# Kernel tuning notes

Measured on AMD Instinct MI355X. Metric: run time of the kernel, lower is better.

## Reference

```python
import jax, jax.numpy as jnp
import numpy as np

B, S, D, H = 4, 4096, 1024, 1024


def log_g(x):
    # where(x >= 0, log(relu(x) + 0.5), -softplus(-x)); relu(x)+0.5 >= 0.5 so log is safe
    return jnp.where(x >= 0, jnp.log(jax.nn.relu(x) + 0.5), -jax.nn.softplus(-x))


def setup_inputs() -> dict:
    key = jax.random.key(0)
    ks = jax.random.split(key, 8)
    scale = 1.0 / np.sqrt(D)
    return {
        "x_t": jax.random.normal(ks[0], (B, S, D), dtype=jnp.float32),
        "pre_h": jax.random.normal(ks[1], (B, 1, H), dtype=jnp.float32),
        "W_f": jax.random.uniform(ks[2], (H, D), jnp.float32, -scale, scale),
        "b_f": jax.random.uniform(ks[3], (H,), jnp.float32, -scale, scale),
        "W_i": jax.random.uniform(ks[4], (H, D), jnp.float32, -scale, scale),
        "b_i": jax.random.uniform(ks[5], (H,), jnp.float32, -scale, scale),
        "W_h": jax.random.uniform(ks[6], (H, D), jnp.float32, -scale, scale),
        "b_h": jax.random.uniform(ks[7], (H,), jnp.float32, -scale, scale),
    }


def reference(x_t, pre_h, W_f, b_f, W_i, b_i, W_h, b_h):
    sp = jax.nn.softplus
    f_pre = jnp.einsum("bsd,hd->bsh", x_t, W_f) + b_f
    i_pre = jnp.einsum("bsd,hd->bsh", x_t, W_i) + b_i
    h_pre = jnp.einsum("bsd,hd->bsh", x_t, W_h) + b_h

    diff = sp(-f_pre) - sp(-i_pre)
    log_f = -sp(diff)        # (B, S, H)
    log_i = -sp(-diff)       # (B, S, H)

    log_h0 = log_g(pre_h)                 # (B, 1, H)
    log_tilde_h = log_g(h_pre)            # (B, S, H)
    log_values = jnp.concatenate([log_h0, log_i + log_tilde_h], axis=1)  # (B, S+1, H)

    # parallel_scan_log: pad cumsum at END of seq dim (as in source: F.pad(..., (0,0,0,1)))
    a_star = jnp.pad(jnp.cumsum(log_f, axis=1), ((0, 0), (0, 1), (0, 0)))  # (B, S+1, H)
    log_h0_plus_b_star = jax.lax.cumlogsumexp(log_values - a_star, axis=1)
    log_h = a_star + log_h0_plus_b_star
    return jnp.exp(log_h)[:, 1:]  # (B, S, H)
```

## Files before the change

### kernel.cpp

```cpp
#include <hip/hip_runtime.h>
#include <hip/hip_bf16.h>
#include <math.h>

#define B_DIM 4
#define S_DIM 4096
#define K_DIM 1024
#define H_DIM 1024
#define M_DIM (B_DIM * S_DIM)

#define BMT 128
#define BNT 64
#define KT_ITERS (K_DIM / 32)

#define NCHUNK 64
#define CLEN (S_DIM / NCHUNK)

typedef __attribute__((ext_vector_type(8))) _Float16 f16x8;
typedef __attribute__((ext_vector_type(4))) _Float16 f16x4;
typedef __attribute__((ext_vector_type(4))) float f32x4;

__device__ __forceinline__ float sp_f(float x) {
    return fmaxf(x, 0.0f) + __logf(1.0f + __expf(-fabsf(x)));
}
__device__ __forceinline__ float log_g_f(float x) {
    return (x >= 0.0f) ? __logf(x + 0.5f) : -sp_f(-x);
}
__device__ __forceinline__ float logaddexp_f(float a, float b) {
    float m = fmaxf(a, b);
    return m + __logf(1.0f + __expf(-fabsf(a - b)));
}
__device__ __forceinline__ float exp_sat(float x) {
    return __expf(fminf(x, 85.0f));
}

__device__ __forceinline__ void gl_lds16(const void* g, void* l) {
    __builtin_amdgcn_global_load_lds(
        (const __attribute__((address_space(1))) unsigned int*)g,
        (__attribute__((address_space(3))) unsigned int*)l, 16, 0, 0);
}

__global__ __launch_bounds__(256) void conv_f16(
    const float* __restrict__ src, _Float16* __restrict__ dst, int n4)
{
    int i = blockIdx.x * 256 + threadIdx.x;
    if (i >= n4) return;
    float4 v = ((const float4*)src)[i];
    f16x4 o = {(_Float16)v.x, (_Float16)v.y, (_Float16)v.z, (_Float16)v.w};
    ((f16x4*)dst)[i] = o;
}

__global__ __launch_bounds__(256, 3) void gemm3(
    const _Float16* __restrict__ xh,
    const _Float16* __restrict__ wh,
    const float* __restrict__ bfp, const float* __restrict__ bip,
    const float* __restrict__ bhp,
    _Float16* __restrict__ lf_out, _Float16* __restrict__ w_out)
{
    __shared__ __align__(16) char smem[20480];

    const int tid = threadIdx.x;
    const int lane = tid & 63;
    const int wv = tid >> 6;
    const int wm = wv >> 1;
    const int wn = wv & 1;

    const int row0 = blockIdx.y * BMT;
    const int col0 = blockIdx.x * BNT;

    const int arow = tid & 127, akq = tid >> 7;
    unsigned ga0 = (unsigned)(((row0 + arow) * K_DIM + akq * 8) * 2);
    const int brow = tid & 63, bkq = tid >> 6;
    unsigned gb0 = (unsigned)(((0 * H_DIM + col0 + brow) * K_DIM + bkq * 8) * 2);
    unsigned gb1 = (unsigned)(((1 * H_DIM + col0 + brow) * K_DIM + bkq * 8) * 2);
    unsigned gb2 = (unsigned)(((2 * H_DIM + col0 + brow) * K_DIM + bkq * 8) * 2);

    const char* __restrict__ px = (const char*)xh;
    const char* __restrict__ pw = (const char*)wh;

    int aoff[4], boff[2];
#pragma unroll
    for (int mi = 0; mi < 4; ++mi)
        aoff[mi] = ((lane >> 4) << 11) + ((wm * 64 + mi * 16 + (lane & 15)) << 4);
#pragma unroll
    for (int nj = 0; nj < 2; ++nj)
        boff[nj] = ((lane >> 4) << 10) + ((wn * 32 + nj * 16 + (lane & 15)) << 4);

    f32x4 acc[3][4][2];
#pragma unroll
    for (int g = 0; g < 3; ++g)
#pragma unroll
        for (int mi = 0; mi < 4; ++mi)
#pragma unroll
            for (int nj = 0; nj < 2; ++nj)
                acc[g][mi][nj] = (f32x4){0.f, 0.f, 0.f, 0.f};

    for (int kt = 0; kt < KT_ITERS; ++kt) {
        __syncthreads();
        gl_lds16(px + ga0, smem + tid * 16);
        gl_lds16(px + ga0 + 32, smem + 4096 + tid * 16);
        gl_lds16(pw + gb0, smem + 8192 + tid * 16);
        gl_lds16(pw + gb1, smem + 12288 + tid * 16);
        gl_lds16(pw + gb2, smem + 16384 + tid * 16);
        ga0 += 64; gb0 += 64; gb1 += 64; gb2 += 64;
        __syncthreads();

        f16x8 a[4];
#pragma unroll
        for (int mi = 0; mi < 4; ++mi)
            a[mi] = *(const f16x8*)(smem + aoff[mi]);
#pragma unroll
        for (int g = 0; g < 3; ++g) {
            const char* bb = smem + 8192 + g * 4096;
            f16x8 b0 = *(const f16x8*)(bb + boff[0]);
            f16x8 b1 = *(const f16x8*)(bb + boff[1]);
#pragma unroll
            for (int mi = 0; mi < 4; ++mi) {
                acc[g][mi][0] = __builtin_amdgcn_mfma_f32_16x16x32_f16(a[mi], b0, acc[g][mi][0], 0, 0, 0);
                acc[g][mi][1] = __builtin_amdgcn_mfma_f32_16x16x32_f16(a[mi], b1, acc[g][mi][1], 0, 0, 0);
            }
        }
    }

    int nidx[2];
    float bfv[2], biv[2], bhv[2];
#pragma unroll
    for (int nj = 0; nj < 2; ++nj) {
        nidx[nj] = col0 + wn * 32 + nj * 16 + (lane & 15);
        bfv[nj] = bfp[nidx[nj]];
        biv[nj] = bip[nidx[nj]];
        bhv[nj] = bhp[nidx[nj]];
    }
#pragma unroll
    for (int mi = 0; mi < 4; ++mi) {
#pragma unroll
        for (int r = 0; r < 4; ++r) {
            int m = row0 + wm * 64 + mi * 16 + ((lane >> 4) << 2) + r;
#pragma unroll
            for (int nj = 0; nj < 2; ++nj) {
                float f_pre = acc[0][mi][nj][r] + bfv[nj];
                float i_pre = acc[1][mi][nj][r] + biv[nj];
                float h_pre = acc[2][mi][nj][r] + bhv[nj];
                float diff = sp_f(-f_pre) - sp_f(-i_pre);
                float lfv = -sp_f(diff);
                float wv_ = -sp_f(-diff) + log_g_f(h_pre);
                size_t o = (size_t)m * H_DIM + nidx[nj];
                lf_out[o] = (_Float16)lfv;
                w_out[o] = (_Float16)wv_;
            }
        }
    }
}

__global__ __launch_bounds__(256) void scan_pass_a(
    const _Float16* __restrict__ lf, const _Float16* __restrict__ w,
    float2* __restrict__ agg)
{
    int tid = blockIdx.x * blockDim.x + threadIdx.x;
    int h = tid & (H_DIM - 1);
    int b = (tid >> 10) & (B_DIM - 1);
    int q = tid >> 12;

    int tstart = q * CLEN + 1;
    int tend = (q == NCHUNK - 1) ? (S_DIM - 1) : (q * CLEN + CLEN);

    size_t idx = (size_t)(b * S_DIM + tstart) * H_DIM + h;
    float c = 0.0f, r = -INFINITY;
    for (int t = tstart; t <= tend; ++t) {
        c += (float)lf[idx];
        r = logaddexp_f(r, (float)w[idx - H_DIM] - c);
        idx += H_DIM;
    }
    agg[(size_t)(b * H_DIM + h) * NCHUNK + q] = make_float2(c, r);
}

__global__ __launch_bounds__(256) void scan_pass_b(
    const _Float16* __restrict__ lf, const float* __restrict__ preh,
    const float2* __restrict__ agg, float2* __restrict__ prefix)
{
    int col = blockIdx.x * blockDim.x + threadIdx.x;
    int h = col & (H_DIM - 1);
    int b = col >> 10;

    float lf0 = (float)lf[(size_t)(b * S_DIM) * H_DIM + h];
    float C = lf0;
    float R = log_g_f(preh[b * H_DIM + h]) - lf0;
    for (int q = 0; q < NCHUNK; ++q) {
        prefix[(size_t)col * NCHUNK + q] = make_float2(C, R);
        float2 a = agg[(size_t)col * NCHUNK + q];
        float Rn = logaddexp_f(R, a.y - C);
        C += a.x;
        R = Rn;
    }
}

__global__ __launch_bounds__(256) void scan_pass_c(
    const _Float16* __restrict__ lf, const _Float16* __restrict__ w,
    const float2* __restrict__ prefix, float* __restrict__ out)
{
    int tid = blockIdx.x * blockDim.x + threadIdx.x;
    int h = tid & (H_DIM - 1);
    int b = (tid >> 10) & (B_DIM - 1);
    int q = tid >> 12;

    float2 p = prefix[(size_t)(b * H_DIM + h) * NCHUNK + q];
    float C = p.x, R = p.y;

    int tstart = q * CLEN + 1;
    int tend = (q == NCHUNK - 1) ? (S_DIM - 1) : (q * CLEN + CLEN);

    size_t idx = (size_t)(b * S_DIM + tstart) * H_DIM + h;
    for (int t = tstart; t <= tend; ++t) {
        C += (float)lf[idx];
        R = logaddexp_f(R, (float)w[idx - H_DIM] - C);
        out[idx - H_DIM] = exp_sat(C + R);
        idx += H_DIM;
    }
    if (q == NCHUNK - 1) {
        R = logaddexp_f(R, (float)w[idx - H_DIM]);
        out[idx - H_DIM] = exp_sat(R);
    }
}

extern "C" void kernel_launch(void* const* d_in, const int* in_sizes, int n_in,
                              void* d_out, int out_size, void* d_ws, size_t ws_size,
                              hipStream_t stream) {
    const float* x    = (const float*)d_in[0];
    const float* preh = (const float*)d_in[1];
    const float* Wf   = (const float*)d_in[2];
    const float* bf   = (const float*)d_in[3];
    const float* Wi   = (const float*)d_in[4];
    const float* bi   = (const float*)d_in[5];
    const float* Wh   = (const float*)d_in[6];
    const float* bh   = (const float*)d_in[7];
    float* out = (float*)d_out;

    _Float16* xh = (_Float16*)d_ws;
    _Float16* wh = xh + (size_t)M_DIM * K_DIM;
    _Float16* lf = wh + (size_t)3 * H_DIM * K_DIM;
    _Float16* wbuf = lf + (size_t)M_DIM * H_DIM;
    float2* agg = (float2*)(wbuf + (size_t)M_DIM * H_DIM);
    float2* prefix = agg + (size_t)B_DIM * H_DIM * NCHUNK;

    conv_f16<<<(M_DIM * K_DIM / 4) / 256, 256, 0, stream>>>(x, xh, M_DIM * K_DIM / 4);
    conv_f16<<<(H_DIM * K_DIM / 4) / 256, 256, 0, stream>>>(Wf, wh, H_DIM * K_DIM / 4);
    conv_f16<<<(H_DIM * K_DIM / 4) / 256, 256, 0, stream>>>(
        Wi, wh + (size_t)H_DIM * K_DIM, H_DIM * K_DIM / 4);
    conv_f16<<<(H_DIM * K_DIM / 4) / 256, 256, 0, stream>>>(
        Wh, wh + (size_t)2 * H_DIM * K_DIM, H_DIM * K_DIM / 4);

    gemm3<<<dim3(H_DIM / BNT, M_DIM / BMT), 256, 0, stream>>>(
        xh, wh, bf, bi, bh, lf, wbuf);

    scan_pass_a<<<(B_DIM * H_DIM * NCHUNK) / 256, 256, 0, stream>>>(lf, wbuf, agg);
    scan_pass_b<<<(B_DIM * H_DIM) / 256, 256, 0, stream>>>(lf, preh, agg, prefix);
    scan_pass_c<<<(B_DIM * H_DIM * NCHUNK) / 256, 256, 0, stream>>>(lf, wbuf, prefix, out);
}
```

Before: 393.0 us.

## Interleave lf/w buffers, widen scan to two columns, double GEMM K tile, fuse conversions

Merges the four fp16 conversion launches into one kernel. Doubles the GEMM K tile per iteration to 64, halving the barrier count at the cost of twice the LDS. Stores log_f and the log-value term interleaved as half2 in a single buffer. The scan passes now handle two hidden columns per thread with wider loads and stores, and carry the previous w value in a register instead of reloading it. These changes target launch overhead, synchronization and memory transaction efficiency, though fewer threads in the scan passes and higher LDS use may reduce occupancy.

```diff
diff --git a/kernel.cpp b/kernel.cpp
--- a/kernel.cpp
+++ b/kernel.cpp
@@ -1,5 +1,4 @@
 #include <hip/hip_runtime.h>
-#include <hip/hip_bf16.h>
 #include <math.h>
 
 #define B_DIM 4
@@ -10,13 +9,16 @@
 
 #define BMT 128
 #define BNT 64
-#define KT_ITERS (K_DIM / 32)
+#define BKT 64
+#define KT_ITERS (K_DIM / BKT)
 
 #define NCHUNK 64
 #define CLEN (S_DIM / NCHUNK)
+#define HP (H_DIM / 2)
 
 typedef __attribute__((ext_vector_type(8))) _Float16 f16x8;
 typedef __attribute__((ext_vector_type(4))) _Float16 f16x4;
+typedef __attribute__((ext_vector_type(2))) _Float16 f16x2;
 typedef __attribute__((ext_vector_type(4))) float f32x4;
 
 __device__ __forceinline__ float sp_f(float x) {
@@ -39,14 +41,22 @@
         (__attribute__((address_space(3))) unsigned int*)l, 16, 0, 0);
 }
 
-__global__ __launch_bounds__(256) void conv_f16(
-    const float* __restrict__ src, _Float16* __restrict__ dst, int n4)
+#define N4X (M_DIM * K_DIM / 4)
+#define N4W (H_DIM * K_DIM / 4)
+__global__ __launch_bounds__(256) void conv_all(
+    const float* __restrict__ x, const float* __restrict__ Wf,
+    const float* __restrict__ Wi, const float* __restrict__ Wh,
+    _Float16* __restrict__ dst)
 {
     int i = blockIdx.x * 256 + threadIdx.x;
-    if (i >= n4) return;
-    float4 v = ((const float4*)src)[i];
-    f16x4 o = {(_Float16)v.x, (_Float16)v.y, (_Float16)v.z, (_Float16)v.w};
-    ((f16x4*)dst)[i] = o;
+    const float* src; int off;
+    if (i < N4X)              { src = x;  off = i; }
+    else if (i < N4X + N4W)   { src = Wf; off = i - N4X; }
+    else if (i < N4X + 2*N4W) { src = Wi; off = i - N4X - N4W; }
+    else                      { src = Wh; off = i - N4X - 2*N4W; }
+    float4 v = ((const float4*)src)[off];
+    ((f16x4*)dst)[i] = (f16x4){(_Float16)v.x, (_Float16)v.y,
+                               (_Float16)v.z, (_Float16)v.w};
 }
 
 __global__ __launch_bounds__(256, 3) void gemm3(
@@ -54,9 +64,9 @@
     const _Float16* __restrict__ wh,
     const float* __restrict__ bfp, const float* __restrict__ bip,
     const float* __restrict__ bhp,
-    _Float16* __restrict__ lf_out, _Float16* __restrict__ w_out)
-{
-    __shared__ __align__(16) char smem[20480];
+    f16x2* __restrict__ lw_out)
+{
+    __shared__ __align__(16) char smem[40960];
 
     const int tid = threadIdx.x;
     const int lane = tid & 63;
@@ -67,12 +77,13 @@
     const int row0 = blockIdx.y * BMT;
     const int col0 = blockIdx.x * BNT;
 
-    const int arow = tid & 127, akq = tid >> 7;
-    unsigned ga0 = (unsigned)(((row0 + arow) * K_DIM + akq * 8) * 2);
-    const int brow = tid & 63, bkq = tid >> 6;
-    unsigned gb0 = (unsigned)(((0 * H_DIM + col0 + brow) * K_DIM + bkq * 8) * 2);
-    unsigned gb1 = (unsigned)(((1 * H_DIM + col0 + brow) * K_DIM + bkq * 8) * 2);
-    unsigned gb2 = (unsigned)(((2 * H_DIM + col0 + brow) * K_DIM + bkq * 8) * 2);
+    const int arow = tid & 127;
+    unsigned ga = (unsigned)((row0 + arow) * (K_DIM * 2) + (tid >> 7) * 16);
+    const int brow = tid & 63;
+    const unsigned bko = (unsigned)((tid >> 6) * 16);
+    unsigned gb0 = (unsigned)((0 * H_DIM + col0 + brow) * (K_DIM * 2)) + bko;
+    unsigned gb1 = (unsigned)((1 * H_DIM + col0 + brow) * (K_DIM * 2)) + bko;
+    unsigned gb2 = (unsigned)((2 * H_DIM + col0 + brow) * (K_DIM * 2)) + bko;
 
     const char* __restrict__ px = (const char*)xh;
     const char* __restrict__ pw = (const char*)wh;
@@ -96,27 +107,36 @@
 
     for (int kt = 0; kt < KT_ITERS; ++kt) {
         __syncthreads();
-        gl_lds16(px + ga0, smem + tid * 16);
-        gl_lds16(px + ga0 + 32, smem + 4096 + tid * 16);
-        gl_lds16(pw + gb0, smem + 8192 + tid * 16);
-        gl_lds16(pw + gb1, smem + 12288 + tid * 16);
-        gl_lds16(pw + gb2, smem + 16384 + tid * 16);
-        ga0 += 64; gb0 += 64; gb1 += 64; gb2 += 64;
+#pragma unroll
+        for (int j = 0; j < 4; ++j)
+            gl_lds16(px + ga + j * 32, smem + j * 4096 + tid * 16);
+#pragma unroll
+        for (int j = 0; j < 2; ++j) {
+            gl_lds16(pw + gb0 + j * 64, smem + 16384 + j * 4096 + tid * 16);
+            gl_lds16(pw + gb1 + j * 64, smem + 24576 + j * 4096 + tid * 16);
+            gl_lds16(pw + gb2 + j * 64, smem + 32768 + j * 4096 + tid * 16);
+        }
+        ga += 128; gb0 += 128; gb1 += 128; gb2 += 128;
         __syncthreads();
 
-        f16x8 a[4];
-#pragma unroll
-        for (int mi = 0; mi < 4; ++mi)
-            a[mi] = *(const f16x8*)(smem + aoff[mi]);
-#pragma unroll
-        for (int g = 0; g < 3; ++g) {
-            const char* bb = smem + 8192 + g * 4096;
-            f16x8 b0 = *(const f16x8*)(bb + boff[0]);
-            f16x8 b1 = *(const f16x8*)(bb + boff[1]);
-#pragma unroll
-            for (int mi = 0; mi < 4; ++mi) {
-                acc[g][mi][0] = __builtin_amdgcn_mfma_f32_16x16x32_f16(a[mi], b0, acc[g][mi][0], 0, 0, 0);
-                acc[g][mi][1] = __builtin_amdgcn_mfma_f32_16x16x32_f16(a[mi], b1, acc[g][mi][1], 0, 0, 0);
+#pragma unroll
+        for (int kk = 0; kk < 2; ++kk) {
+            const int ao = kk * 8192;
+            const int bo = kk * 4096;
+            f16x8 a[4];
+#pragma unroll
+            for (int mi = 0; mi < 4; ++mi)
+                a[mi] = *(const f16x8*)(smem + ao + aoff[mi]);
+#pragma unroll
+            for (int g = 0; g < 3; ++g) {
+                const char* bb = smem + 16384 + g * 8192 + bo;
+                f16x8 b0 = *(const f16x8*)(bb + boff[0]);
+                f16x8 b1 = *(const f16x8*)(bb + boff[1]);
+#pragma unroll
+                for (int mi = 0; mi < 4; ++mi) {
+                    acc[g][mi][0] = __builtin_amdgcn_mfma_f32_16x16x32_f16(a[mi], b0, acc[g][mi][0], 0, 0, 0);
+                    acc[g][mi][1] = __builtin_amdgcn_mfma_f32_16x16x32_f16(a[mi], b1, acc[g][mi][1], 0, 0, 0);
+                }
             }
         }
     }
@@ -143,81 +163,102 @@
                 float diff = sp_f(-f_pre) - sp_f(-i_pre);
                 float lfv = -sp_f(diff);
                 float wv_ = -sp_f(-diff) + log_g_f(h_pre);
-                size_t o = (size_t)m * H_DIM + nidx[nj];
-                lf_out[o] = (_Float16)lfv;
-                w_out[o] = (_Float16)wv_;
+                lw_out[(size_t)m * H_DIM + nidx[nj]] =
+                    (f16x2){(_Float16)lfv, (_Float16)wv_};
             }
         }
     }
 }
 
 __global__ __launch_bounds__(256) void scan_pass_a(
-    const _Float16* __restrict__ lf, const _Float16* __restrict__ w,
-    float2* __restrict__ agg)
-{
-    int tid = blockIdx.x * blockDim.x + threadIdx.x;
-    int h = tid & (H_DIM - 1);
-    int b = (tid >> 10) & (B_DIM - 1);
-    int q = tid >> 12;
+    const f16x2* __restrict__ lw, float4* __restrict__ agg4)
+{
+    int t0 = blockIdx.x * 256 + threadIdx.x;
+    int hp = t0 & (HP - 1);
+    int b = (t0 >> 9) & (B_DIM - 1);
+    int q = t0 >> 11;
+    int h0 = hp * 2;
 
     int tstart = q * CLEN + 1;
     int tend = (q == NCHUNK - 1) ? (S_DIM - 1) : (q * CLEN + CLEN);
 
-    size_t idx = (size_t)(b * S_DIM + tstart) * H_DIM + h;
-    float c = 0.0f, r = -INFINITY;
+    size_t idx = (size_t)(b * S_DIM + tstart - 1) * H_DIM + h0;
+    f16x4 v = *(const f16x4*)(lw + idx);
+    float wp0 = (float)v[1], wp1 = (float)v[3];
+    float c0 = 0.f, c1 = 0.f, r0 = -INFINITY, r1 = -INFINITY;
     for (int t = tstart; t <= tend; ++t) {
-        c += (float)lf[idx];
-        r = logaddexp_f(r, (float)w[idx - H_DIM] - c);
         idx += H_DIM;
-    }
-    agg[(size_t)(b * H_DIM + h) * NCHUNK + q] = make_float2(c, r);
+        v = *(const f16x4*)(lw + idx);
+        c0 += (float)v[0];
+        c1 += (float)v[2];
+        r0 = logaddexp_f(r0, wp0 - c0);
+        r1 = logaddexp_f(r1, wp1 - c1);
+        wp0 = (float)v[1];
+        wp1 = (float)v[3];
+    }
+    agg4[(size_t)(b * HP + hp) * NCHUNK + q] = make_float4(c0, r0, c1, r1);
 }
 
 __global__ __launch_bounds__(256) void scan_pass_b(
-    const _Float16* __restrict__ lf, const float* __restrict__ preh,
-    const float2* __restrict__ agg, float2* __restrict__ prefix)
-{
-    int col = blockIdx.x * blockDim.x + threadIdx.x;
-    int h = col & (H_DIM - 1);
-    int b = col >> 10;
-
-    float lf0 = (float)lf[(size_t)(b * S_DIM) * H_DIM + h];
-    float C = lf0;
-    float R = log_g_f(preh[b * H_DIM + h]) - lf0;
+    const f16x2* __restrict__ lw, const float* __restrict__ preh,
+    const float4* __restrict__ agg4, float4* __restrict__ prefix4)
+{
+    int t0 = blockIdx.x * 256 + threadIdx.x;
+    int hp = t0 & (HP - 1);
+    int b = t0 >> 9;
+    int h0 = hp * 2;
+
+    f16x4 v = *(const f16x4*)(lw + (size_t)(b * S_DIM) * H_DIM + h0);
+    float lf00 = (float)v[0], lf01 = (float)v[2];
+    float C0 = lf00, C1 = lf01;
+    float R0 = log_g_f(preh[b * H_DIM + h0]) - lf00;
+    float R1 = log_g_f(preh[b * H_DIM + h0 + 1]) - lf01;
+    size_t base = (size_t)(b * HP + hp) * NCHUNK;
     for (int q = 0; q < NCHUNK; ++q) {
-        prefix[(size_t)col * NCHUNK + q] = make_float2(C, R);
-        float2 a = agg[(size_t)col * NCHUNK + q];
-        float Rn = logaddexp_f(R, a.y - C);
-        C += a.x;
-        R = Rn;
+        prefix4[base + q] = make_float4(C0, R0, C1, R1);
+        float4 a = agg4[base + q];
+        float Rn0 = logaddexp_f(R0, a.y - C0);
+        float Rn1 = logaddexp_f(R1, a.w - C1);
+        C0 += a.x; C1 += a.z;
+        R0 = Rn0; R1 = Rn1;
     }
 }
 
 __global__ __launch_bounds__(256) void scan_pass_c(
-    const _Float16* __restrict__ lf, const _Float16* __restrict__ w,
-    const float2* __restrict__ prefix, float* __restrict__ out)
-{
-    int tid = blockIdx.x * blockDim.x + threadIdx.x;
-    int h = tid & (H_DIM - 1);
-    int b = (tid >> 10) & (B_DIM - 1);
-    int q = tid >> 12;
-
-    float2 p = prefix[(size_t)(b * H_DIM + h) * NCHUNK + q];
-    float C = p.x, R = p.y;
+    const f16x2* __restrict__ lw, const float4* __restrict__ prefix4,
+    float* __restrict__ out)
+{
+    int t0 = blockIdx.x * 256 + threadIdx.x;
+    int hp = t0 & (HP - 1);
+    int b = (t0 >> 9) & (B_DIM - 1);
+    int q = t0 >> 11;
+    int h0 = hp * 2;
+
+    float4 p = prefix4[(size_t)(b * HP + hp) * NCHUNK + q];
+    float C0 = p.x, R0 = p.y, C1 = p.z, R1 = p.w;
 
     int tstart = q * CLEN + 1;
     int tend = (q == NCHUNK - 1) ? (S_DIM - 1) : (q * CLEN + CLEN);
 
-    size_t idx = (size_t)(b * S_DIM + tstart) * H_DIM + h;
+    size_t idx = (size_t)(b * S_DIM + tstart - 1) * H_DIM + h0;
+    f16x4 v = *(const f16x4*)(lw + idx);
+    float wp0 = (float)v[1], wp1 = (float)v[3];
     for (int t = tstart; t <= tend; ++t) {
-        C += (float)lf[idx];
-        R = logaddexp_f(R, (float)w[idx - H_DIM] - C);
-        out[idx - H_DIM] = exp_sat(C + R);
         idx += H_DIM;
+        v = *(const f16x4*)(lw + idx);
+        C0 += (float)v[0];
+        C1 += (float)v[2];
+        R0 = logaddexp_f(R0, wp0 - C0);
+        R1 = logaddexp_f(R1, wp1 - C1);
+        *(float2*)(out + idx - H_DIM) = make_float2(exp_sat(C0 + R0),
+                                                    exp_sat(C1 + R1));
+        wp0 = (float)v[1];
+        wp1 = (float)v[3];
     }
     if (q == NCHUNK - 1) {
-        R = logaddexp_f(R, (float)w[idx - H_DIM]);
-        out[idx - H_DIM] = exp_sat(R);
+        R0 = logaddexp_f(R0, wp0);
+        R1 = logaddexp_f(R1, wp1);
+        *(float2*)(out + idx) = make_float2(exp_sat(R0), exp_sat(R1));
     }
 }
 
@@ -236,22 +277,16 @@
 
     _Float16* xh = (_Float16*)d_ws;
     _Float16* wh = xh + (size_t)M_DIM * K_DIM;
-    _Float16* lf = wh + (size_t)3 * H_DIM * K_DIM;
-    _Float16* wbuf = lf + (size_t)M_DIM * H_DIM;
-    float2* agg = (float2*)(wbuf + (size_t)M_DIM * H_DIM);
-    float2* prefix = agg + (size_t)B_DIM * H_DIM * NCHUNK;
-
-    conv_f16<<<(M_DIM * K_DIM / 4) / 256, 256, 0, stream>>>(x, xh, M_DIM * K_DIM / 4);
-    conv_f16<<<(H_DIM * K_DIM / 4) / 256, 256, 0, stream>>>(Wf, wh, H_DIM * K_DIM / 4);
-    conv_f16<<<(H_DIM * K_DIM / 4) / 256, 256, 0, stream>>>(
-        Wi, wh + (size_t)H_DIM * K_DIM, H_DIM * K_DIM / 4);
-    conv_f16<<<(H_DIM * K_DIM / 4) / 256, 256, 0, stream>>>(
-        Wh, wh + (size_t)2 * H_DIM * K_DIM, H_DIM * K_DIM / 4);
+    f16x2* lw = (f16x2*)(wh + (size_t)3 * H_DIM * K_DIM);
+    float4* agg4 = (float4*)(lw + (size_t)M_DIM * H_DIM);
+    float4* prefix4 = agg4 + (size_t)B_DIM * HP * NCHUNK;
+
+    conv_all<<<(N4X + 3 * N4W) / 256, 256, 0, stream>>>(x, Wf, Wi, Wh, xh);
 
     gemm3<<<dim3(H_DIM / BNT, M_DIM / BMT), 256, 0, stream>>>(
-        xh, wh, bf, bi, bh, lf, wbuf);
-
-    scan_pass_a<<<(B_DIM * H_DIM * NCHUNK) / 256, 256, 0, stream>>>(lf, wbuf, agg);
-    scan_pass_b<<<(B_DIM * H_DIM) / 256, 256, 0, stream>>>(lf, preh, agg, prefix);
-    scan_pass_c<<<(B_DIM * H_DIM * NCHUNK) / 256, 256, 0, stream>>>(lf, wbuf, prefix, out);
-}
+        xh, wh, bf, bi, bh, lw);
+
+    scan_pass_a<<<(B_DIM * HP * NCHUNK) / 256, 256, 0, stream>>>(lw, agg4);
+    scan_pass_b<<<(B_DIM * HP) / 256, 256, 0, stream>>>(lw, preh, agg4, prefix4);
+    scan_pass_c<<<(B_DIM * HP * NCHUNK) / 256, 256, 0, stream>>>(lw, prefix4, out);
+}
```

Measured after the change: 399.1 us. Within noise of the previous version (+1.6%).
